# Kernel optimization log

Measured on AMD Instinct MI355X. Metric: run time of the kernel, lower is better.

## Reference

```python
import jax, jax.numpy as jnp
import numpy as np

NUM_CLASSES = 80
CONF_THRE = 0.2
NMS_THRE = 0.45
MAX_DET = 300   # fixed cap replacing torch's variable-length NMS output (padded + keep mask)
IMG = 640.0


def setup_inputs() -> dict:
    key = jax.random.key(0)
    k1, k2 = jax.random.split(key)
    pred = jax.random.uniform(k1, (32, 8400, 85), dtype=jnp.float32)
    # scale cx,cy,w,h to pixel range so IoU/NMS geometry is realistic
    pred = pred.at[..., :4].multiply(IMG)
    zone = jax.random.uniform(k2, (8, 2), dtype=jnp.float32) * IMG
    return {"prediction": pred, "zone": zone}


def _pairwise_iou(b):
    # b: [B, K, 4] in x1y1x2y2
    area = jnp.clip(b[..., 2] - b[..., 0], 0.0) * jnp.clip(b[..., 3] - b[..., 1], 0.0)
    lt = jnp.maximum(b[:, :, None, :2], b[:, None, :, :2])
    rb = jnp.minimum(b[:, :, None, 2:], b[:, None, :, 2:])
    wh = jnp.clip(rb - lt, 0.0)
    inter = wh[..., 0] * wh[..., 1]
    return inter / (area[:, :, None] + area[:, None, :] - inter + 1e-9)


def _postprocess(prediction):
    # decode cx,cy,w,h -> x1,y1,x2,y2
    xy = prediction[..., :2]
    wh = prediction[..., 2:4]
    boxes = jnp.concatenate([xy - wh * 0.5, xy + wh * 0.5], axis=-1)  # [B,N,4]
    obj = prediction[..., 4]                                           # [B,N]
    cls = prediction[..., 5:5 + NUM_CLASSES]
    class_conf = jnp.max(cls, axis=-1)                                 # [B,N]
    class_pred = jnp.argmax(cls, axis=-1)                              # [B,N]

    # confidence mask (obj * class_conf >= thre); invalid -> -inf so top_k drops them
    nms_score = obj * class_conf
    nms_score = jnp.where(nms_score >= CONF_THRE, nms_score, -jnp.inf)

    s, idx = jax.lax.top_k(nms_score, MAX_DET)                         # [B,K]
    b = jnp.take_along_axis(boxes, idx[..., None], axis=1)             # [B,K,4]

    # class-agnostic greedy NMS on score-sorted boxes (matches torchvision.ops.nms)
    iou = _pairwise_iou(b)                                             # [B,K,K]
    keep = jnp.isfinite(s)                                             # valid (passed conf) entries
    ar = jnp.arange(MAX_DET)
    def body(i, keep):
        sup = keep[:, i][:, None] & (iou[:, i, :] > NMS_THRE) & (ar > i)
        return keep & jnp.logical_not(sup)
    keep = jax.lax.fori_loop(0, MAX_DET, body, keep)

    obj_s = jnp.take_along_axis(obj, idx, axis=1)
    conf_s = jnp.take_along_axis(class_conf, idx, axis=1)
    cls_s = jnp.take_along_axis(class_pred, idx, axis=1).astype(jnp.int32)
    # extract_boxes_scores_and_classes: score = max over columns [obj, class_conf]
    scores = jnp.maximum(obj_s, conf_s)
    return b, scores, cls_s, keep


def _points_inside_zone(px, py, zone):
    # px, py: [B,K]; zone: [Z,2]. Ray-casting parity test (faithful to torch version).
    zr = jnp.roll(zone, shift=1, axis=0)
    xi, yi = zone[:, 0], zone[:, 1]
    xj, yj = zr[:, 0], zr[:, 1]
    pyb = py[..., None]  # [B,K,1] vs [Z]
    pxb = px[..., None]
    gyi = yi > pyb
    gyj = yj > pyb
    gx = (xj - xi) * (pyb - yi) / (yj - yi) + xi
    inter = (gyi != gyj) & (gx > pxb)
    return (jnp.sum(inter.astype(jnp.int32), axis=-1) % 2) > 0


def reference(prediction, zone):
    b, scores, classes, keep = _postprocess(prediction)
    cx = (b[..., 0] + b[..., 2]) * 0.5
    cy = (b[..., 1] + b[..., 3]) * 0.5
    in_zone = _points_inside_zone(cx, cy, zone) & keep
    centers_yx = jnp.stack([cy, cx], axis=-1)                          # [B,K,2]
    boxes_yxyx = jnp.stack([b[..., 1], b[..., 0], b[..., 3], b[..., 2]], axis=-1)
    return boxes_yxyx, in_zone, scores, classes, centers_yx, keep
```

## Files before the change

### kernel.cpp

```cpp
#include <hip/hip_runtime.h>
#include <stdint.h>

typedef unsigned long long ull;

#define NA 8400
#define NB 32
#define KTOP 300
#define NC 80
#define TB 512
#define CH 17
#define NKPAD 8704
#define NBIN 309
#define HSTR 311
#define NCPY 8
#define BASEK 0xBE4CCCCDu
#define CANDMAX 256

#define O1 38400
#define O2 48000
#define O3 57600
#define O4 67200
#define O5 86400

#define WS_BATCH_BASE (2u << 20)
#define WS_BATCH_STRIDE 8192

__global__ __launch_bounds__(256) void score_kernel(const float* __restrict__ pred,
                                                    uint32_t* __restrict__ keys) {
    __shared__ float sP[128 * 85];
    const int blk = blockIdx.x;
    const float4* g4 = (const float4*)(pred + (size_t)blk * 128 * 85);
    float4* l4 = (float4*)sP;
    for (int i = threadIdx.x; i < (128 * 85 / 4); i += 256) l4[i] = g4[i];
    __syncthreads();
    const int t = threadIdx.x;
    if (t < 128) {
        const float* p = sP + t * 85;
        float obj = p[4];
        float b0 = p[5], b1 = p[6], b2 = p[7], b3 = p[8];
        #pragma unroll
        for (int c = 4; c < NC; c += 4) {
            b0 = fmaxf(b0, p[5 + c]);
            b1 = fmaxf(b1, p[6 + c]);
            b2 = fmaxf(b2, p[7 + c]);
            b3 = fmaxf(b3, p[8 + c]);
        }
        float best = fmaxf(fmaxf(b0, b1), fmaxf(b2, b3));
        float sc = obj * best;
        uint32_t u = (sc >= 0.2f) ? (__float_as_uint(sc) | 0x80000000u) : 0x007FFFFFu;
        keys[(size_t)blk * 128 + t] = u;
    }
}

__device__ __forceinline__ uint32_t key_bin(uint32_t k) {
    return (k < BASEK) ? 0u : (1u + ((k - BASEK) >> 16));
}

__global__ __launch_bounds__(TB) void select_kernel(const float* __restrict__ pred,
                                                    const uint32_t* __restrict__ keys,
                                                    uint8_t* __restrict__ ws,
                                                    float* __restrict__ out) {
    #pragma clang fp contract(off)
    __shared__ uint32_t sKeys[NKPAD];
    __shared__ uint32_t sH[NCPY * HSTR];
    __shared__ ull sSel[KTOP];
    __shared__ ull sSorted[KTOP];
    __shared__ ull sCand[CANDMAX];
    __shared__ uint32_t sWTot[8];
    __shared__ uint32_t sBc[2];
    __shared__ uint32_t sRank[KTOP];
    __shared__ uint32_t sCN;

    const int b = blockIdx.x;
    const int t = threadIdx.x;
    const int lane = t & 63;
    const int wv = t >> 6;

    {
        const uint4* g4 = (const uint4*)(keys + (size_t)b * NA);
        uint4* l4 = (uint4*)sKeys;
        for (int i = t; i < NA / 4; i += TB) l4[i] = g4[i];
        for (int i = NA + t; i < NKPAD; i += TB) sKeys[i] = 0u;
    }
    for (int i = t; i < NCPY * HSTR; i += TB) sH[i] = 0u;
    if (t < KTOP) sRank[t] = 0u;
    __syncthreads();

    const int beg = t * CH;
    {
        uint32_t* hw = &sH[wv * HSTR];
        #pragma unroll
        for (int e = 0; e < CH; ++e) {
            uint32_t k = sKeys[beg + e];
            atomicAdd(&hw[key_bin(k)], 1u);
        }
    }
    __syncthreads();

    uint32_t v = 0, s = 0;
    if (t < 320) {
        if (t < NBIN) {
            #pragma unroll
            for (int c = 0; c < NCPY; ++c) v += sH[c * HSTR + t];
        }
        s = v;
        #pragma unroll
        for (int off = 1; off < 64; off <<= 1) {
            uint32_t o = __shfl_down(s, off, 64);
            if (lane + off < 64) s += o;
        }
        if (lane == 0) sWTot[wv] = s;
    }
    __syncthreads();
    if (t < 320) {
        uint32_t S = s;
        for (int w2 = wv + 1; w2 < 5; ++w2) S += sWTot[w2];
        uint32_t above = S - v;
        if (above < KTOP && S >= KTOP) {
            sBc[0] = (uint32_t)t;
            sBc[1] = KTOP - above;
        }
    }
    __syncthreads();
    const uint32_t Tbin = sBc[0];
    const uint32_t rem = sBc[1];
    const uint32_t cntgt = KTOP - rem;

    {
        uint32_t gtc = 0, eqc = 0;
        #pragma unroll
        for (int e = 0; e < CH; ++e) {
            uint32_t bin = key_bin(sKeys[beg + e]);
            gtc += (bin > Tbin) ? 1u : 0u;
            eqc += (bin == Tbin) ? 1u : 0u;
        }
        uint32_t pack = (gtc << 16) | eqc;
        uint32_t ps = pack;
        #pragma unroll
        for (int off = 1; off < 64; off <<= 1) {
            uint32_t o = __shfl_up(ps, off, 64);
            if (lane >= off) ps += o;
        }
        if (lane == 63) sWTot[wv] = ps;
        __syncthreads();
        uint32_t excl = ps - pack;
        #pragma unroll
        for (int w2 = 0; w2 < 8; ++w2) if (w2 < wv) excl += sWTot[w2];
        uint32_t gtoff = excl >> 16;
        uint32_t eqoff = excl & 0xFFFFu;
        if (t == TB - 1) {
            uint32_t tot = eqoff + eqc;
            sCN = (tot > CANDMAX) ? CANDMAX : tot;
        }
        #pragma unroll
        for (int e = 0; e < CH; ++e) {
            uint32_t k = sKeys[beg + e];
            uint32_t bin = key_bin(k);
            uint32_t idx = (uint32_t)(beg + e);
            if (bin > Tbin) {
                sSel[gtoff++] = ((ull)k << 32) | (ull)(0xFFFFFFFFu - idx);
            } else if (bin == Tbin) {
                if (eqoff < CANDMAX)
                    sCand[eqoff] = ((ull)k << 32) | (ull)(0xFFFFFFFFu - idx);
                eqoff++;
            }
        }
        __syncthreads();
    }

    {
        int cn = (int)sCN;
        if (t < cn) {
            ull my = sCand[t];
            uint32_t rk = 0;
            for (int j = 0; j < cn; ++j) rk += (sCand[j] > my) ? 1u : 0u;
            if (rk < rem) sSel[cntgt + rk] = my;
        }
        __syncthreads();
    }

    for (int p2 = t; p2 < KTOP * 4; p2 += TB) {
        const int i = p2 >> 2;
        const int q = p2 & 3;
        const ull my = sSel[i];
        const int j0 = q * 75, j1 = j0 + 75;
        uint32_t cnt = 0;
        for (int j = j0; j < j1; ++j)
            cnt += (sSel[j] > my) ? 1u : 0u;
        if (cnt) atomicAdd(&sRank[i], cnt);
    }
    __syncthreads();
    if (t < KTOP) sSorted[sRank[t]] = sSel[t];
    __syncthreads();

    ull* selW = (ull*)(ws + WS_BATCH_BASE + (size_t)b * WS_BATCH_STRIDE);
    float* boxW = (float*)(selW + KTOP);
    const size_t bo = (size_t)b * KTOP;
    if (t < KTOP) selW[t] = sSorted[t];
    for (int tt = t; tt < 2 * KTOP; tt += TB) {
        const int row = tt >> 1;
        const int half = tt & 1;
        const uint32_t a = 0xFFFFFFFFu - (uint32_t)sSorted[row];
        const float* p = pred + ((size_t)b * NA + a) * 85;
        const int cbase = half * 40;
        float v0 = p[5 + cbase], v1 = p[6 + cbase], v2 = p[7 + cbase], v3 = p[8 + cbase];
        int   c0 = cbase, c1 = cbase + 1, c2 = cbase + 2, c3 = cbase + 3;
        #pragma unroll
        for (int c = 4; c < 40; c += 4) {
            float w0 = p[5 + cbase + c],     w1 = p[6 + cbase + c];
            float w2 = p[7 + cbase + c],     w3 = p[8 + cbase + c];
            if (w0 > v0) { v0 = w0; c0 = cbase + c; }
            if (w1 > v1) { v1 = w1; c1 = cbase + c + 1; }
            if (w2 > v2) { v2 = w2; c2 = cbase + c + 2; }
            if (w3 > v3) { v3 = w3; c3 = cbase + c + 3; }
        }
        float bv = v0; int bc = c0;
        if (v1 > bv || (v1 == bv && c1 < bc)) { bv = v1; bc = c1; }
        if (v2 > bv || (v2 == bv && c2 < bc)) { bv = v2; bc = c2; }
        if (v3 > bv || (v3 == bv && c3 < bc)) { bv = v3; bc = c3; }
        float pv = __shfl_xor(bv, 1, 64);
        int   pc = __shfl_xor(bc, 1, 64);
        if (half == 0) {
            if (pv > bv) { bv = pv; bc = pc; }
            float x = p[0], y = p[1], w = p[2], h = p[3], obj = p[4];
            float hw = w * 0.5f, hh = h * 0.5f;
            float x1 = x - hw, y1 = y - hh, x2 = x + hw, y2 = y + hh;
            boxW[row] = x1; boxW[KTOP + row] = y1;
            boxW[2 * KTOP + row] = x2; boxW[3 * KTOP + row] = y2;
            out[(bo + row) * 4 + 0] = y1;
            out[(bo + row) * 4 + 1] = x1;
            out[(bo + row) * 4 + 2] = y2;
            out[(bo + row) * 4 + 3] = x2;
            out[O4 + (bo + row) * 2 + 0] = (y1 + y2) * 0.5f;
            out[O4 + (bo + row) * 2 + 1] = (x1 + x2) * 0.5f;
            out[O2 + bo + row] = fmaxf(obj, bv);
            out[O3 + bo + row] = (float)bc;
        }
    }
}

__global__ __launch_bounds__(TB) void nms_kernel(const float* __restrict__ zone,
                                                 const uint8_t* __restrict__ ws,
                                                 float* __restrict__ out) {
    #pragma clang fp contract(off)
    __shared__ float sB0[KTOP], sB1[KTOP], sB2[KTOP], sB3[KTOP];
    __shared__ ull sMask[KTOP * 5];
    __shared__ ull sSel[KTOP];
    __shared__ uint32_t sPar[KTOP];
    __shared__ ull sKeepF[5];
    __shared__ float sZone[16];
    const int b = blockIdx.x;
    const int t = threadIdx.x;
    const int lane = t & 63;
    const int wv = t >> 6;
    const ull* selG = (const ull*)(ws + WS_BATCH_BASE + (size_t)b * WS_BATCH_STRIDE);
    const float* boxG = (const float*)(selG + KTOP);
    if (t < KTOP) {
        sSel[t] = selG[t];
        sB0[t] = boxG[t];            sB1[t] = boxG[KTOP + t];
        sB2[t] = boxG[2 * KTOP + t]; sB3[t] = boxG[3 * KTOP + t];
    }
    if (t < 16) sZone[t] = zone[t];
    __syncthreads();

    for (int p2 = t; p2 < KTOP * 5; p2 += TB) {
        const int role = p2 / KTOP;
        const int i = p2 - role * KTOP;
        const int j0 = role * 64;
        int jmax = j0 + 64; if (jmax > KTOP) jmax = KTOP;
        if (jmax <= i + 1) { sMask[i * 5 + role] = 0ull; continue; }
        float x1 = sB0[i], y1 = sB1[i], x2 = sB2[i], y2 = sB3[i];
        float ai = fmaxf(x2 - x1, 0.0f) * fmaxf(y2 - y1, 0.0f);
        ull bits = 0ull;
        for (int j = j0; j < jmax; ++j) {
            float bx1 = sB0[j], by1 = sB1[j], bx2 = sB2[j], by2 = sB3[j];
            float aj = fmaxf(bx2 - bx1, 0.0f) * fmaxf(by2 - by1, 0.0f);
            float iw = fminf(x2, bx2) - fmaxf(x1, bx1); iw = fmaxf(iw, 0.0f);
            float ih = fminf(y2, by2) - fmaxf(y1, by1); ih = fmaxf(ih, 0.0f);
            float inter = iw * ih;
            float den = ai + aj;
            den = den - inter;
            den = den + 1e-9f;
            float iou = inter / den;
            if (j > i && iou > 0.45f) bits |= (1ull << (j - j0));
        }
        sMask[i * 5 + role] = bits;
    }
    __syncthreads();

    const size_t bo = (size_t)b * KTOP;
    if (wv == 0) {
        ull rm[5][5];
        ull kw[5];
        #pragma unroll
        for (int w = 0; w < 5; ++w) {
            int i = w * 64 + lane;
            bool f = (i < KTOP) && (((uint32_t)(sSel[i] >> 32)) > 0x007FFFFFu);
            kw[w] = __ballot(f);
            #pragma unroll
            for (int ww = 0; ww < 5; ++ww)
                rm[w][ww] = (i < KTOP) ? sMask[i * 5 + ww] : 0ull;
        }
        #pragma unroll
        for (int w = 0; w < 5; ++w) {
            ull cur = kw[w];
            while (cur) {
                int ib = __builtin_ctzll(cur);
                ull m0 = __shfl(rm[w][0], ib);
                ull m1 = __shfl(rm[w][1], ib);
                ull m2 = __shfl(rm[w][2], ib);
                ull m3 = __shfl(rm[w][3], ib);
                ull m4 = __shfl(rm[w][4], ib);
                kw[0] &= ~m0; kw[1] &= ~m1; kw[2] &= ~m2; kw[3] &= ~m3; kw[4] &= ~m4;
                ull done = (ib == 63) ? 0ull : (~0ull << (ib + 1));
                cur = kw[w] & done;
            }
        }
        if (lane == 0) {
            #pragma unroll
            for (int w = 0; w < 5; ++w) sKeepF[w] = kw[w];
        }
    } else if (t >= 64 && t < 64 + KTOP) {
        const int i = t - 64;
        float cy = (sB1[i] + sB3[i]) * 0.5f;
        float cx = (sB0[i] + sB2[i]) * 0.5f;
        int cnt = 0;
        #pragma unroll
        for (int e = 0; e < 8; ++e) {
            float xi = sZone[2 * e], yi = sZone[2 * e + 1];
            int ep = (e + 7) & 7;
            float xj = sZone[2 * ep], yj = sZone[2 * ep + 1];
            bool gyi = yi > cy, gyj = yj > cy;
            if (gyi != gyj) {
                float gx = (xj - xi) * (cy - yi) / (yj - yi) + xi;
                if (gx > cx) cnt++;
            }
        }
        sPar[i] = (uint32_t)(cnt & 1);
    }
    __syncthreads();

    if (t < KTOP) {
        int kp = (int)((sKeepF[t >> 6] >> (t & 63)) & 1ull);
        int inz = (sPar[t] && kp) ? 1 : 0;
        out[O1 + bo + t] = (float)inz;
        out[O5 + bo + t] = (float)kp;
    }
}

extern "C" void kernel_launch(void* const* d_in, const int* in_sizes, int n_in,
                              void* d_out, int out_size, void* d_ws, size_t ws_size,
                              hipStream_t stream) {
    const float* pred = (const float*)d_in[0];
    const float* zone = (const float*)d_in[1];
    float* out = (float*)d_out;
    uint32_t* keys = (uint32_t*)d_ws;
    uint8_t* ws = (uint8_t*)d_ws;

    score_kernel<<<(NB * NA) / 128, 256, 0, stream>>>(pred, keys);
    select_kernel<<<NB, TB, 0, stream>>>(pred, keys, ws, out);
    nms_kernel<<<NB, TB, 0, stream>>>(zone, ws, out);
}
```

Measured before the change: 193.6 us.

## Fuse select and NMS kernels, keep keys in registers, merge ranking into gather

Merges the top-k selection and NMS kernels into one per-batch kernel, so the workspace round trip for sorted keys and boxes and one launch are gone. Each thread now holds its keys in registers using a strided layout instead of staging 8400 keys through shared memory. The separate rank-sort pass is folded into the class-argmax gather loop, and results are scattered directly to their sorted positions. CANDMAX is raised to 512, which adds shared memory for the candidate buffer and more work in the quadratic candidate ranking when the threshold bin is crowded.

```diff
diff --git a/kernel.cpp b/kernel.cpp
--- a/kernel.cpp
+++ b/kernel.cpp
@@ -9,21 +9,17 @@
 #define NC 80
 #define TB 512
 #define CH 17
-#define NKPAD 8704
 #define NBIN 309
 #define HSTR 311
 #define NCPY 8
 #define BASEK 0xBE4CCCCDu
-#define CANDMAX 256
+#define CANDMAX 512
 
 #define O1 38400
 #define O2 48000
 #define O3 57600
 #define O4 67200
 #define O5 86400
-
-#define WS_BATCH_BASE (2u << 20)
-#define WS_BATCH_STRIDE 8192
 
 __global__ __launch_bounds__(256) void score_kernel(const float* __restrict__ pred,
                                                     uint32_t* __restrict__ keys) {
@@ -56,19 +52,22 @@
     return (k < BASEK) ? 0u : (1u + ((k - BASEK) >> 16));
 }
 
-__global__ __launch_bounds__(TB) void select_kernel(const float* __restrict__ pred,
-                                                    const uint32_t* __restrict__ keys,
-                                                    uint8_t* __restrict__ ws,
-                                                    float* __restrict__ out) {
+__global__ __launch_bounds__(TB) void batch_kernel(const float* __restrict__ pred,
+                                                   const float* __restrict__ zone,
+                                                   const uint32_t* __restrict__ keys,
+                                                   float* __restrict__ out) {
     #pragma clang fp contract(off)
-    __shared__ uint32_t sKeys[NKPAD];
     __shared__ uint32_t sH[NCPY * HSTR];
     __shared__ ull sSel[KTOP];
     __shared__ ull sSorted[KTOP];
     __shared__ ull sCand[CANDMAX];
+    __shared__ float sB0[KTOP], sB1[KTOP], sB2[KTOP], sB3[KTOP];
+    __shared__ ull sMask[KTOP * 5];
     __shared__ uint32_t sWTot[8];
     __shared__ uint32_t sBc[2];
-    __shared__ uint32_t sRank[KTOP];
+    __shared__ uint32_t sPar[KTOP];
+    __shared__ ull sKeepF[5];
+    __shared__ float sZone[16];
     __shared__ uint32_t sCN;
 
     const int b = blockIdx.x;
@@ -76,24 +75,21 @@
     const int lane = t & 63;
     const int wv = t >> 6;
 
-    {
-        const uint4* g4 = (const uint4*)(keys + (size_t)b * NA);
-        uint4* l4 = (uint4*)sKeys;
-        for (int i = t; i < NA / 4; i += TB) l4[i] = g4[i];
-        for (int i = NA + t; i < NKPAD; i += TB) sKeys[i] = 0u;
+    uint32_t myk[CH];
+    #pragma unroll
+    for (int e = 0; e < CH; ++e) {
+        int idx = e * TB + t;
+        myk[e] = (idx < NA) ? keys[(size_t)b * NA + idx] : 0u;
     }
     for (int i = t; i < NCPY * HSTR; i += TB) sH[i] = 0u;
-    if (t < KTOP) sRank[t] = 0u;
-    __syncthreads();
-
-    const int beg = t * CH;
+    if (t < 16) sZone[t] = zone[t];
+    __syncthreads();
+
     {
         uint32_t* hw = &sH[wv * HSTR];
         #pragma unroll
-        for (int e = 0; e < CH; ++e) {
-            uint32_t k = sKeys[beg + e];
-            atomicAdd(&hw[key_bin(k)], 1u);
-        }
+        for (int e = 0; e < CH; ++e)
+            atomicAdd(&hw[key_bin(myk[e])], 1u);
     }
     __syncthreads();
 
@@ -130,7 +126,7 @@
         uint32_t gtc = 0, eqc = 0;
         #pragma unroll
         for (int e = 0; e < CH; ++e) {
-            uint32_t bin = key_bin(sKeys[beg + e]);
+            uint32_t bin = key_bin(myk[e]);
             gtc += (bin > Tbin) ? 1u : 0u;
             eqc += (bin == Tbin) ? 1u : 0u;
         }
@@ -154,9 +150,9 @@
         }
         #pragma unroll
         for (int e = 0; e < CH; ++e) {
-            uint32_t k = sKeys[beg + e];
+            uint32_t k = myk[e];
             uint32_t bin = key_bin(k);
-            uint32_t idx = (uint32_t)(beg + e);
+            uint32_t idx = (uint32_t)(e * TB + t);
             if (bin > Tbin) {
                 sSel[gtoff++] = ((ull)k << 32) | (ull)(0xFFFFFFFFu - idx);
             } else if (bin == Tbin) {
@@ -179,28 +175,12 @@
         __syncthreads();
     }
 
-    for (int p2 = t; p2 < KTOP * 4; p2 += TB) {
-        const int i = p2 >> 2;
-        const int q = p2 & 3;
-        const ull my = sSel[i];
-        const int j0 = q * 75, j1 = j0 + 75;
-        uint32_t cnt = 0;
-        for (int j = j0; j < j1; ++j)
-            cnt += (sSel[j] > my) ? 1u : 0u;
-        if (cnt) atomicAdd(&sRank[i], cnt);
-    }
-    __syncthreads();
-    if (t < KTOP) sSorted[sRank[t]] = sSel[t];
-    __syncthreads();
-
-    ull* selW = (ull*)(ws + WS_BATCH_BASE + (size_t)b * WS_BATCH_STRIDE);
-    float* boxW = (float*)(selW + KTOP);
     const size_t bo = (size_t)b * KTOP;
-    if (t < KTOP) selW[t] = sSorted[t];
     for (int tt = t; tt < 2 * KTOP; tt += TB) {
         const int row = tt >> 1;
         const int half = tt & 1;
-        const uint32_t a = 0xFFFFFFFFu - (uint32_t)sSorted[row];
+        const ull selv = sSel[row];
+        const uint32_t a = 0xFFFFFFFFu - (uint32_t)selv;
         const float* p = pred + ((size_t)b * NA + a) * 85;
         const int cbase = half * 40;
         float v0 = p[5 + cbase], v1 = p[6 + cbase], v2 = p[7 + cbase], v3 = p[8 + cbase];
@@ -214,53 +194,35 @@
             if (w2 > v2) { v2 = w2; c2 = cbase + c + 2; }
             if (w3 > v3) { v3 = w3; c3 = cbase + c + 3; }
         }
+        uint32_t rk = 0;
+        const int jb = half * 150;
+        for (int j = jb; j < jb + 150; ++j)
+            rk += (sSel[j] > selv) ? 1u : 0u;
         float bv = v0; int bc = c0;
         if (v1 > bv || (v1 == bv && c1 < bc)) { bv = v1; bc = c1; }
         if (v2 > bv || (v2 == bv && c2 < bc)) { bv = v2; bc = c2; }
         if (v3 > bv || (v3 == bv && c3 < bc)) { bv = v3; bc = c3; }
         float pv = __shfl_xor(bv, 1, 64);
         int   pc = __shfl_xor(bc, 1, 64);
+        uint32_t rko = __shfl_xor(rk, 1, 64);
+        const uint32_t rank = rk + rko;
         if (half == 0) {
             if (pv > bv) { bv = pv; bc = pc; }
             float x = p[0], y = p[1], w = p[2], h = p[3], obj = p[4];
             float hw = w * 0.5f, hh = h * 0.5f;
             float x1 = x - hw, y1 = y - hh, x2 = x + hw, y2 = y + hh;
-            boxW[row] = x1; boxW[KTOP + row] = y1;
-            boxW[2 * KTOP + row] = x2; boxW[3 * KTOP + row] = y2;
-            out[(bo + row) * 4 + 0] = y1;
-            out[(bo + row) * 4 + 1] = x1;
-            out[(bo + row) * 4 + 2] = y2;
-            out[(bo + row) * 4 + 3] = x2;
-            out[O4 + (bo + row) * 2 + 0] = (y1 + y2) * 0.5f;
-            out[O4 + (bo + row) * 2 + 1] = (x1 + x2) * 0.5f;
-            out[O2 + bo + row] = fmaxf(obj, bv);
-            out[O3 + bo + row] = (float)bc;
-        }
-    }
-}
-
-__global__ __launch_bounds__(TB) void nms_kernel(const float* __restrict__ zone,
-                                                 const uint8_t* __restrict__ ws,
-                                                 float* __restrict__ out) {
-    #pragma clang fp contract(off)
-    __shared__ float sB0[KTOP], sB1[KTOP], sB2[KTOP], sB3[KTOP];
-    __shared__ ull sMask[KTOP * 5];
-    __shared__ ull sSel[KTOP];
-    __shared__ uint32_t sPar[KTOP];
-    __shared__ ull sKeepF[5];
-    __shared__ float sZone[16];
-    const int b = blockIdx.x;
-    const int t = threadIdx.x;
-    const int lane = t & 63;
-    const int wv = t >> 6;
-    const ull* selG = (const ull*)(ws + WS_BATCH_BASE + (size_t)b * WS_BATCH_STRIDE);
-    const float* boxG = (const float*)(selG + KTOP);
-    if (t < KTOP) {
-        sSel[t] = selG[t];
-        sB0[t] = boxG[t];            sB1[t] = boxG[KTOP + t];
-        sB2[t] = boxG[2 * KTOP + t]; sB3[t] = boxG[3 * KTOP + t];
-    }
-    if (t < 16) sZone[t] = zone[t];
+            sSorted[rank] = selv;
+            sB0[rank] = x1; sB1[rank] = y1; sB2[rank] = x2; sB3[rank] = y2;
+            out[(bo + rank) * 4 + 0] = y1;
+            out[(bo + rank) * 4 + 1] = x1;
+            out[(bo + rank) * 4 + 2] = y2;
+            out[(bo + rank) * 4 + 3] = x2;
+            out[O4 + (bo + rank) * 2 + 0] = (y1 + y2) * 0.5f;
+            out[O4 + (bo + rank) * 2 + 1] = (x1 + x2) * 0.5f;
+            out[O2 + bo + rank] = fmaxf(obj, bv);
+            out[O3 + bo + rank] = (float)bc;
+        }
+    }
     __syncthreads();
 
     for (int p2 = t; p2 < KTOP * 5; p2 += TB) {
@@ -288,14 +250,13 @@
     }
     __syncthreads();
 
-    const size_t bo = (size_t)b * KTOP;
     if (wv == 0) {
         ull rm[5][5];
         ull kw[5];
         #pragma unroll
         for (int w = 0; w < 5; ++w) {
             int i = w * 64 + lane;
-            bool f = (i < KTOP) && (((uint32_t)(sSel[i] >> 32)) > 0x007FFFFFu);
+            bool f = (i < KTOP) && (((uint32_t)(sSorted[i] >> 32)) > 0x007FFFFFu);
             kw[w] = __ballot(f);
             #pragma unroll
             for (int ww = 0; ww < 5; ++ww)
@@ -355,9 +316,7 @@
     const float* zone = (const float*)d_in[1];
     float* out = (float*)d_out;
     uint32_t* keys = (uint32_t*)d_ws;
-    uint8_t* ws = (uint8_t*)d_ws;
 
     score_kernel<<<(NB * NA) / 128, 256, 0, stream>>>(pred, keys);
-    select_kernel<<<NB, TB, 0, stream>>>(pred, keys, ws, out);
-    nms_kernel<<<NB, TB, 0, stream>>>(zone, ws, out);
+    batch_kernel<<<NB, TB, 0, stream>>>(pred, zone, keys, out);
 }
```

After: 185.7 us. 4.1% less time.
